# Performance work log

Measured on AMD Instinct MI355X. Metric: run time of the kernel, lower is better.

## Reference

```python
import jax, jax.numpy as jnp
import numpy as np

FP8_MAX = 448.0   # torch.finfo(float8_e4m3fn).max
BLK = 128         # block_size = [128, 128] for weights; [1, 128] for activations
E, H, I, T, TOPK = 8, 2048, 1408, 512, 2
FP8 = jnp.float8_e4m3fn


def fp8_round(x):
    """Round-trip through float8_e4m3fn (simulates .to(float8_e4m3fn))."""
    return jnp.clip(x, -FP8_MAX, FP8_MAX).astype(FP8).astype(jnp.float32)


def setup_inputs() -> dict:
    key = jax.random.key(0)
    ks = jax.random.split(key, 7)
    hidden_states = jax.random.normal(ks[0], (T, H), jnp.float32)
    top_k_index = jax.random.randint(ks[1], (T, TOPK), 0, E)
    top_k_weights = jax.random.uniform(ks[2], (T, TOPK), jnp.float32)
    # FP8 weight codes (stored as fp32 values exactly representable in e4m3fn)
    gate_up_proj = fp8_round(jax.random.normal(ks[3], (E, 2 * I, H), jnp.float32))
    gate_up_proj_scale_inv = jax.random.uniform(ks[4], (E, (2 * I) // BLK, H // BLK), jnp.float32, 1e-4, 1e-2)
    down_proj = fp8_round(jax.random.normal(ks[5], (E, H, I), jnp.float32))
    down_proj_scale_inv = jax.random.uniform(ks[6], (E, H // BLK, I // BLK), jnp.float32, 1e-4, 1e-2)
    return {
        "hidden_states": hidden_states,
        "top_k_index": top_k_index,
        "top_k_weights": top_k_weights,
        "gate_up_proj": gate_up_proj,
        "gate_up_proj_scale_inv": gate_up_proj_scale_inv,
        "down_proj": down_proj,
        "down_proj_scale_inv": down_proj_scale_inv,
    }


def dequant_weight(wq, s):
    # wq: [E, N, K] fp8 codes; s: [E, N//BLK, K//BLK] per-128x128-block scale_inv
    e, n, k = wq.shape
    wb = wq.reshape(e, n // BLK, BLK, k // BLK, BLK)
    return (wb * s[:, :, None, :, None]).reshape(e, n, k)


def quant_dequant_act(x):
    # dynamic per-(row, 128-block) fp8 activation quantization, then dequant
    shp = x.shape
    xb = x.reshape(shp[:-1] + (shp[-1] // BLK, BLK))
    amax = jnp.max(jnp.abs(xb), axis=-1, keepdims=True)
    scale = jnp.maximum(amax, 1e-12) / FP8_MAX
    q = fp8_round(xb / scale)
    return (q * scale).reshape(shp)


def reference(hidden_states, top_k_index, top_k_weights, gate_up_proj,
              gate_up_proj_scale_inv, down_proj, down_proj_scale_inv):
    w_gu = dequant_weight(gate_up_proj, gate_up_proj_scale_inv)  # [E, 2I, H]
    w_d = dequant_weight(down_proj, down_proj_scale_inv)         # [E, H, I]
    # activation quantization is per-token-block, so unrouted tokens are
    # unaffected; dense per-expert compute + combine-weight mask equals the
    # original gather/scatter loop exactly (unrouted contributions weight 0).
    x = quant_dequant_act(hidden_states)                         # [T, H]
    gate_up = jnp.einsum('th,enh->etn', x, w_gu)                 # [E, T, 2I]
    gate, up = jnp.split(gate_up, 2, axis=-1)
    h = jax.nn.silu(gate) * up                                   # [E, T, I]
    h = quant_dequant_act(h)
    down = jnp.einsum('eti,ehi->eth', h, w_d)                    # [E, T, H]
    # combine[t, e] = sum over top-k slots routing token t to expert e
    combine = jnp.sum(jax.nn.one_hot(top_k_index, E, dtype=top_k_weights.dtype)
                      * top_k_weights[..., None], axis=1)        # [T, E]
    out = jnp.einsum('eth,te->th', down, combine)
    return out.astype(hidden_states.dtype)
```

## Files before the change

kernel.cpp:

```cpp
#include <hip/hip_runtime.h>
#include <math.h>

#define NE 8
#define HD 2048
#define ID 1408
#define NT 512
#define FP8MAX 448.0f

typedef __attribute__((ext_vector_type(4))) float floatx4;

__device__ __forceinline__ floatx4 fzero4() {
    floatx4 z; z.x = 0.f; z.y = 0.f; z.z = 0.f; z.w = 0.f; return z;
}

#define OFF_OFFS  0
#define OFF_TOK   1024
#define OFF_WGT   8192
#define OFF_ENT   16384
#define OFF_XSG   32768
#define OFF_XG    131072
#define OFF_HS    (3*1024*1024)
#define OFF_HQ    (3*1024*1024 + 65536)
#define OFF_GU0   (5*1024*1024)
#define OFF_GU1   (17*1024*1024)

#define LDA 136

__global__ void route_kernel(const int* __restrict__ tki,
                             const float* __restrict__ tkw,
                             int* __restrict__ offs,
                             int* __restrict__ tok,
                             float* __restrict__ wgt,
                             int* __restrict__ ent) {
    __shared__ int cnt[NE];
    __shared__ int cur[NE];
    __shared__ int base[NE + 1];
    int tid = threadIdx.x;
    if (tid < NE) { cnt[tid] = 0; cur[tid] = 0; }
    __syncthreads();
    int e = tki[tid];
    atomicAdd(&cnt[e], 1);
    __syncthreads();
    if (tid == 0) {
        int s = 0;
        for (int i = 0; i < NE; i++) { base[i] = s; s += cnt[i]; }
        base[NE] = s;
    }
    __syncthreads();
    int pos = atomicAdd(&cur[e], 1);
    int j = base[e] + pos;
    tok[j] = tid >> 1;
    wgt[j] = tkw[tid];
    ent[tid] = j;
    if (tid <= NE) offs[tid] = base[tid];
}

__global__ void quant_x_kernel(const float* __restrict__ x,
                               const int* __restrict__ ent,
                               unsigned char* __restrict__ xg,
                               float* __restrict__ xsg) {
    int wid = (blockIdx.x * 256 + threadIdx.x) >> 6;
    int lane = threadIdx.x & 63;
    int t = wid >> 4;
    int b = wid & 15;
    const float2 v = *(const float2*)(x + (long)t * HD + b * 128 + lane * 2);
    float am = fmaxf(fabsf(v.x), fabsf(v.y));
    #pragma unroll
    for (int m = 32; m; m >>= 1) am = fmaxf(am, __shfl_xor(am, m));
    float scale = fmaxf(am, 1e-12f) / FP8MAX;
    int p = __builtin_amdgcn_cvt_pk_fp8_f32(v.x / scale, v.y / scale, 0, false);
    unsigned short pk = (unsigned short)(p & 0xffff);
    int e0 = ent[2 * t], e1 = ent[2 * t + 1];
    *(unsigned short*)(xg + (long)e0 * HD + b * 128 + lane * 2) = pk;
    *(unsigned short*)(xg + (long)e1 * HD + b * 128 + lane * 2) = pk;
    if (lane == 0) { xsg[e0 * 16 + b] = scale; xsg[e1 * 16 + b] = scale; }
}

__global__ void quant_h_kernel(const float* __restrict__ gu0,
                               const float* __restrict__ gu1,
                               unsigned char* __restrict__ hq,
                               float* __restrict__ hs) {
    int wid = (blockIdx.x * 256 + threadIdx.x) >> 6;
    int lane = threadIdx.x & 63;
    int j = wid / 11;
    int b = wid - j * 11;
    long base = (long)j * 2816 + b * 128 + lane * 2;
    float2 ga = *(const float2*)(gu0 + base);
    float2 gb = *(const float2*)(gu1 + base);
    float2 ua = *(const float2*)(gu0 + base + 1408);
    float2 ub = *(const float2*)(gu1 + base + 1408);
    float gx = ga.x + gb.x, gy = ga.y + gb.y;
    float ux = ua.x + ub.x, uy = ua.y + ub.y;
    float hx = (gx / (1.0f + expf(-gx))) * ux;
    float hy = (gy / (1.0f + expf(-gy))) * uy;
    float am = fmaxf(fabsf(hx), fabsf(hy));
    #pragma unroll
    for (int m = 32; m; m >>= 1) am = fmaxf(am, __shfl_xor(am, m));
    float scale = fmaxf(am, 1e-12f) / FP8MAX;
    int p = __builtin_amdgcn_cvt_pk_fp8_f32(hx / scale, hy / scale, 0, false);
    *(unsigned short*)(hq + (long)j * ID + b * 128 + lane * 2) =
        (unsigned short)(p & 0xffff);
    if (lane == 0) hs[j * 11 + b] = scale;
}

__global__ __launch_bounds__(256, 4) void gemm1_kernel(
    const unsigned char* __restrict__ xg,
    const float* __restrict__ xsg,
    const float* __restrict__ wgu,
    const float* __restrict__ sgu,
    const int* __restrict__ offs,
    float* __restrict__ gu0,
    float* __restrict__ gu1) {
    int e = blockIdx.z;
    int jb = blockIdx.x >> 1;
    int kh = blockIdx.x & 1;
    int o0 = offs[e], o1 = offs[e + 1];
    int ne = o1 - o0;
    if (ne <= 0) return;

    __shared__ __align__(16) unsigned char Asm[128 * LDA];
    __shared__ __align__(16) unsigned char Bsm[64 * LDA];
    __shared__ __align__(16) float sxa[128 * 20];

    int tid = threadIdx.x;
    int wave = tid >> 6;
    int lane = tid & 63;
    int lr = lane & 15;
    int lq = lane >> 4;

    int bcol = tid & 31;
    int brow0 = tid >> 5;
    const float* bG = wgu + ((long)e * 2816 + jb * 32 + brow0) * HD + bcol * 4;
    const float* bU = wgu + ((long)e * 2816 + 1408 + jb * 32 + brow0) * HD + bcol * 4;
    const float* sgp = sgu + (e * 22 + (jb >> 2)) * 16;
    const float* sup = sgu + (e * 22 + 11 + (jb >> 2)) * 16;

    int aseg = tid & 7;
    int arow0 = tid >> 3;
    int kbS = kh * 8, kbE = kbS + 8;

    for (int m0 = 0; m0 < ne; m0 += 128) {
        int rem = ne - m0;
        int j0 = o0 + m0;

        {
            int r = tid >> 1, q = tid & 1;
            int j = j0 + r; if (j >= o1) j = o0;
            float4 s0 = *(const float4*)(xsg + j * 16 + q * 8);
            float4 s1 = *(const float4*)(xsg + j * 16 + q * 8 + 4);
            *(float4*)&sxa[r * 20 + q * 8] = s0;
            *(float4*)&sxa[r * 20 + q * 8 + 4] = s1;
        }

        const unsigned char* aBase0;
        const unsigned char* aBase1;
        const unsigned char* aBase2;
        const unsigned char* aBase3;
        {
            int j;
            j = j0 + arow0;       if (j >= o1) j = o0; aBase0 = xg + (long)j * HD + aseg * 16;
            j = j0 + 32 + arow0;  if (j >= o1) j = o0; aBase1 = xg + (long)j * HD + aseg * 16;
            j = j0 + 64 + arow0;  if (j >= o1) j = o0; aBase2 = xg + (long)j * HD + aseg * 16;
            j = j0 + 96 + arow0;  if (j >= o1) j = o0; aBase3 = xg + (long)j * HD + aseg * 16;
        }

        floatx4 facc[8];
        #pragma unroll
        for (int i = 0; i < 8; i++) facc[i] = fzero4();

        for (int kb = kbS; kb < kbE; kb++) {
            {
                uint4 a0 = *(const uint4*)(aBase0 + kb * 128);
                uint4 a1 = *(const uint4*)(aBase1 + kb * 128);
                uint4 a2 = *(const uint4*)(aBase2 + kb * 128);
                uint4 a3 = *(const uint4*)(aBase3 + kb * 128);
                float4 f0 = *(const float4*)(bG + kb * 128);
                float4 f1 = *(const float4*)(bG + kb * 128 + 8 * HD);
                float4 f2 = *(const float4*)(bG + kb * 128 + 16 * HD);
                float4 f3 = *(const float4*)(bG + kb * 128 + 24 * HD);
                float4 f4 = *(const float4*)(bU + kb * 128);
                float4 f5 = *(const float4*)(bU + kb * 128 + 8 * HD);
                float4 f6 = *(const float4*)(bU + kb * 128 + 16 * HD);
                float4 f7 = *(const float4*)(bU + kb * 128 + 24 * HD);
                *(uint4*)(&Asm[(arow0)      * LDA + aseg * 16]) = a0;
                *(uint4*)(&Asm[(arow0 + 32) * LDA + aseg * 16]) = a1;
                *(uint4*)(&Asm[(arow0 + 64) * LDA + aseg * 16]) = a2;
                *(uint4*)(&Asm[(arow0 + 96) * LDA + aseg * 16]) = a3;
                int p0 = __builtin_amdgcn_cvt_pk_fp8_f32(f0.x, f0.y, 0, false);
                p0 = __builtin_amdgcn_cvt_pk_fp8_f32(f0.z, f0.w, p0, true);
                int p1 = __builtin_amdgcn_cvt_pk_fp8_f32(f1.x, f1.y, 0, false);
                p1 = __builtin_amdgcn_cvt_pk_fp8_f32(f1.z, f1.w, p1, true);
                int p2 = __builtin_amdgcn_cvt_pk_fp8_f32(f2.x, f2.y, 0, false);
                p2 = __builtin_amdgcn_cvt_pk_fp8_f32(f2.z, f2.w, p2, true);
                int p3 = __builtin_amdgcn_cvt_pk_fp8_f32(f3.x, f3.y, 0, false);
                p3 = __builtin_amdgcn_cvt_pk_fp8_f32(f3.z, f3.w, p3, true);
                int p4 = __builtin_amdgcn_cvt_pk_fp8_f32(f4.x, f4.y, 0, false);
                p4 = __builtin_amdgcn_cvt_pk_fp8_f32(f4.z, f4.w, p4, true);
                int p5 = __builtin_amdgcn_cvt_pk_fp8_f32(f5.x, f5.y, 0, false);
                p5 = __builtin_amdgcn_cvt_pk_fp8_f32(f5.z, f5.w, p5, true);
                int p6 = __builtin_amdgcn_cvt_pk_fp8_f32(f6.x, f6.y, 0, false);
                p6 = __builtin_amdgcn_cvt_pk_fp8_f32(f6.z, f6.w, p6, true);
                int p7 = __builtin_amdgcn_cvt_pk_fp8_f32(f7.x, f7.y, 0, false);
                p7 = __builtin_amdgcn_cvt_pk_fp8_f32(f7.z, f7.w, p7, true);
                *(unsigned int*)(&Bsm[(brow0)      * LDA + bcol * 4]) = (unsigned int)p0;
                *(unsigned int*)(&Bsm[(brow0 + 8)  * LDA + bcol * 4]) = (unsigned int)p1;
                *(unsigned int*)(&Bsm[(brow0 + 16) * LDA + bcol * 4]) = (unsigned int)p2;
                *(unsigned int*)(&Bsm[(brow0 + 24) * LDA + bcol * 4]) = (unsigned int)p3;
                *(unsigned int*)(&Bsm[(brow0 + 32) * LDA + bcol * 4]) = (unsigned int)p4;
                *(unsigned int*)(&Bsm[(brow0 + 40) * LDA + bcol * 4]) = (unsigned int)p5;
                *(unsigned int*)(&Bsm[(brow0 + 48) * LDA + bcol * 4]) = (unsigned int)p6;
                *(unsigned int*)(&Bsm[(brow0 + 56) * LDA + bcol * 4]) = (unsigned int)p7;
            }
            __syncthreads();
            floatx4 cacc[8];
            #pragma unroll
            for (int i = 0; i < 8; i++) cacc[i] = fzero4();
            #pragma unroll
            for (int ks = 0; ks < 4; ks++) {
                long a[2], b[4];
                #pragma unroll
                for (int mi = 0; mi < 2; mi++)
                    a[mi] = *(const long*)(&Asm[(wave * 32 + mi * 16 + lr) * LDA + ks * 32 + lq * 8]);
                #pragma unroll
                for (int ni = 0; ni < 4; ni++)
                    b[ni] = *(const long*)(&Bsm[(ni * 16 + lr) * LDA + ks * 32 + lq * 8]);
                #pragma unroll
                for (int mi = 0; mi < 2; mi++)
                    #pragma unroll
                    for (int ni = 0; ni < 4; ni++)
                        cacc[mi * 4 + ni] = __builtin_amdgcn_mfma_f32_16x16x32_fp8_fp8(
                            a[mi], b[ni], cacc[mi * 4 + ni], 0, 0, 0);
            }
            float sg = sgp[kb];
            float su = sup[kb];
            #pragma unroll
            for (int mi = 0; mi < 2; mi++) {
                #pragma unroll
                for (int reg = 0; reg < 4; reg++) {
                    float sx = sxa[(wave * 32 + mi * 16 + lq * 4 + reg) * 20 + kb];
                    #pragma unroll
                    for (int ni = 0; ni < 4; ni++) {
                        float sw = (ni < 2) ? sg : su;
                        facc[mi * 4 + ni][reg] += cacc[mi * 4 + ni][reg] * (sw * sx);
                    }
                }
            }
            __syncthreads();
        }

        float* gu = kh ? gu1 : gu0;
        #pragma unroll
        for (int mi = 0; mi < 2; mi++) {
            #pragma unroll
            for (int ni = 0; ni < 4; ni++) {
                #pragma unroll
                for (int reg = 0; reg < 4; reg++) {
                    int r = wave * 32 + mi * 16 + lq * 4 + reg;
                    if (r < rem) {
                        long base = (long)(j0 + r) * 2816;
                        long col = (ni < 2) ? (jb * 32 + ni * 16 + lr)
                                            : (1408 + jb * 32 + (ni - 2) * 16 + lr);
                        gu[base + col] = facc[mi * 4 + ni][reg];
                    }
                }
            }
        }
    }
}

__global__ __launch_bounds__(256, 4) void gemm2_kernel(
    const unsigned char* __restrict__ hq,
    const float* __restrict__ hs,
    const float* __restrict__ wd,
    const float* __restrict__ sd,
    const int* __restrict__ offs,
    float* __restrict__ d0,
    float* __restrict__ d1) {
    int e = blockIdx.z;
    int jb = blockIdx.x >> 1;
    int kh = blockIdx.x & 1;
    int o0 = offs[e], o1 = offs[e + 1];
    int ne = o1 - o0;
    if (ne <= 0) return;

    __shared__ __align__(16) unsigned char Asm[128 * LDA];
    __shared__ __align__(16) unsigned char Bsm[32 * LDA];
    __shared__ __align__(16) float sha[128 * 12];

    int tid = threadIdx.x;
    int wave = tid >> 6;
    int lane = tid & 63;
    int lr = lane & 15;
    int lq = lane >> 4;

    int aseg = tid & 7;
    int arow0 = tid >> 3;

    int bcol = tid & 31;
    int brow0 = tid >> 5;
    const float* bB = wd + ((long)e * HD + jb * 32 + brow0) * ID + bcol * 4;
    const float* sdp = sd + (e * 16 + (jb >> 2)) * 11;

    int kb0 = kh ? 6 : 0, kb1 = kh ? 11 : 6;
    float* dp = kh ? d1 : d0;

    for (int m0 = 0; m0 < ne; m0 += 128) {
        int rem = ne - m0;
        int j0 = o0 + m0;

        if (tid < 128) {
            int j = j0 + tid;
            if (j >= o1) j = o0;
            const float* s = hs + j * 11;
            #pragma unroll
            for (int k = 0; k < 11; k++) sha[tid * 12 + k] = s[k];
        }

        const unsigned char* aBase0;
        const unsigned char* aBase1;
        const unsigned char* aBase2;
        const unsigned char* aBase3;
        {
            int j;
            j = j0 + arow0;       if (j >= o1) j = o0; aBase0 = hq + (long)j * ID + aseg * 16;
            j = j0 + 32 + arow0;  if (j >= o1) j = o0; aBase1 = hq + (long)j * ID + aseg * 16;
            j = j0 + 64 + arow0;  if (j >= o1) j = o0; aBase2 = hq + (long)j * ID + aseg * 16;
            j = j0 + 96 + arow0;  if (j >= o1) j = o0; aBase3 = hq + (long)j * ID + aseg * 16;
        }

        floatx4 facc[4];
        #pragma unroll
        for (int i = 0; i < 4; i++) facc[i] = fzero4();

        for (int kb = kb0; kb < kb1; kb++) {
            {
                uint4 a0 = *(const uint4*)(aBase0 + kb * 128);
                uint4 a1 = *(const uint4*)(aBase1 + kb * 128);
                uint4 a2 = *(const uint4*)(aBase2 + kb * 128);
                uint4 a3 = *(const uint4*)(aBase3 + kb * 128);
                float4 f0 = *(const float4*)(bB + kb * 128);
                float4 f1 = *(const float4*)(bB + kb * 128 + 8 * ID);
                float4 f2 = *(const float4*)(bB + kb * 128 + 16 * ID);
                float4 f3 = *(const float4*)(bB + kb * 128 + 24 * ID);
                *(uint4*)(&Asm[(arow0)      * LDA + aseg * 16]) = a0;
                *(uint4*)(&Asm[(arow0 + 32) * LDA + aseg * 16]) = a1;
                *(uint4*)(&Asm[(arow0 + 64) * LDA + aseg * 16]) = a2;
                *(uint4*)(&Asm[(arow0 + 96) * LDA + aseg * 16]) = a3;
                int p0 = __builtin_amdgcn_cvt_pk_fp8_f32(f0.x, f0.y, 0, false);
                p0 = __builtin_amdgcn_cvt_pk_fp8_f32(f0.z, f0.w, p0, true);
                int p1 = __builtin_amdgcn_cvt_pk_fp8_f32(f1.x, f1.y, 0, false);
                p1 = __builtin_amdgcn_cvt_pk_fp8_f32(f1.z, f1.w, p1, true);
                int p2 = __builtin_amdgcn_cvt_pk_fp8_f32(f2.x, f2.y, 0, false);
                p2 = __builtin_amdgcn_cvt_pk_fp8_f32(f2.z, f2.w, p2, true);
                int p3 = __builtin_amdgcn_cvt_pk_fp8_f32(f3.x, f3.y, 0, false);
                p3 = __builtin_amdgcn_cvt_pk_fp8_f32(f3.z, f3.w, p3, true);
                *(unsigned int*)(&Bsm[(brow0)      * LDA + bcol * 4]) = (unsigned int)p0;
                *(unsigned int*)(&Bsm[(brow0 + 8)  * LDA + bcol * 4]) = (unsigned int)p1;
                *(unsigned int*)(&Bsm[(brow0 + 16) * LDA + bcol * 4]) = (unsigned int)p2;
                *(unsigned int*)(&Bsm[(brow0 + 24) * LDA + bcol * 4]) = (unsigned int)p3;
            }
            __syncthreads();
            floatx4 cacc[4];
            #pragma unroll
            for (int i = 0; i < 4; i++) cacc[i] = fzero4();
            #pragma unroll
            for (int ks = 0; ks < 4; ks++) {
                long a[2], b[2];
                #pragma unroll
                for (int mi = 0; mi < 2; mi++)
                    a[mi] = *(const long*)(&Asm[(wave * 32 + mi * 16 + lr) * LDA + ks * 32 + lq * 8]);
                #pragma unroll
                for (int ni = 0; ni < 2; ni++)
                    b[ni] = *(const long*)(&Bsm[(ni * 16 + lr) * LDA + ks * 32 + lq * 8]);
                #pragma unroll
                for (int mi = 0; mi < 2; mi++)
                    #pragma unroll
                    for (int ni = 0; ni < 2; ni++)
                        cacc[mi * 2 + ni] = __builtin_amdgcn_mfma_f32_16x16x32_fp8_fp8(
                            a[mi], b[ni], cacc[mi * 2 + ni], 0, 0, 0);
            }
            float sw = sdp[kb];
            #pragma unroll
            for (int mi = 0; mi < 2; mi++) {
                #pragma unroll
                for (int reg = 0; reg < 4; reg++) {
                    float sh = sha[(wave * 32 + mi * 16 + lq * 4 + reg) * 12 + kb];
                    #pragma unroll
                    for (int ni = 0; ni < 2; ni++)
                        facc[mi * 2 + ni][reg] += cacc[mi * 2 + ni][reg] * (sw * sh);
                }
            }
            __syncthreads();
        }

        #pragma unroll
        for (int mi = 0; mi < 2; mi++) {
            #pragma unroll
            for (int ni = 0; ni < 2; ni++) {
                #pragma unroll
                for (int reg = 0; reg < 4; reg++) {
                    int r = wave * 32 + mi * 16 + lq * 4 + reg;
                    if (r < rem) {
                        dp[(long)(j0 + r) * HD + jb * 32 + ni * 16 + lr] =
                            facc[mi * 2 + ni][reg];
                    }
                }
            }
        }
    }
}

__global__ void combine_kernel(const float* __restrict__ d0,
                               const float* __restrict__ d1,
                               const int* __restrict__ ent,
                               const float* __restrict__ tkw,
                               float* __restrict__ out) {
    int gid = blockIdx.x * 256 + threadIdx.x;
    int t = gid >> 9;
    int c4 = gid & 511;
    int j0 = ent[2 * t], j1 = ent[2 * t + 1];
    float w0 = tkw[2 * t], w1 = tkw[2 * t + 1];
    long b0 = (long)j0 * HD + c4 * 4;
    long b1 = (long)j1 * HD + c4 * 4;
    float4 a0 = *(const float4*)(d0 + b0);
    float4 a1 = *(const float4*)(d1 + b0);
    float4 a2 = *(const float4*)(d0 + b1);
    float4 a3 = *(const float4*)(d1 + b1);
    float4 r;
    r.x = w0 * (a0.x + a1.x) + w1 * (a2.x + a3.x);
    r.y = w0 * (a0.y + a1.y) + w1 * (a2.y + a3.y);
    r.z = w0 * (a0.z + a1.z) + w1 * (a2.z + a3.z);
    r.w = w0 * (a0.w + a1.w) + w1 * (a2.w + a3.w);
    *(float4*)(out + (long)t * HD + c4 * 4) = r;
}

extern "C" void kernel_launch(void* const* d_in, const int* in_sizes, int n_in,
                              void* d_out, int out_size, void* d_ws, size_t ws_size,
                              hipStream_t stream) {
    (void)in_sizes; (void)n_in; (void)out_size; (void)ws_size;
    const float* x   = (const float*)d_in[0];
    const int*   tki = (const int*)d_in[1];
    const float* tkw = (const float*)d_in[2];
    const float* wgu = (const float*)d_in[3];
    const float* sgu = (const float*)d_in[4];
    const float* wd  = (const float*)d_in[5];
    const float* sd  = (const float*)d_in[6];
    float* out = (float*)d_out;
    char* ws = (char*)d_ws;

    int*   offs = (int*)(ws + OFF_OFFS);
    int*   tok  = (int*)(ws + OFF_TOK);
    float* wgt  = (float*)(ws + OFF_WGT);
    int*   ent  = (int*)(ws + OFF_ENT);
    float* xsg  = (float*)(ws + OFF_XSG);
    unsigned char* xg = (unsigned char*)(ws + OFF_XG);
    float* hs   = (float*)(ws + OFF_HS);
    unsigned char* hq = (unsigned char*)(ws + OFF_HQ);
    float* gu0  = (float*)(ws + OFF_GU0);
    float* gu1  = (float*)(ws + OFF_GU1);
    float* dp0  = (float*)(ws + OFF_GU0);
    float* dp1  = (float*)(ws + OFF_GU1);

    route_kernel<<<1, 1024, 0, stream>>>(tki, tkw, offs, tok, wgt, ent);
    quant_x_kernel<<<2048, 256, 0, stream>>>(x, ent, xg, xsg);
    gemm1_kernel<<<dim3(88, 1, NE), 256, 0, stream>>>(xg, xsg, wgu, sgu, offs, gu0, gu1);
    quant_h_kernel<<<2816, 256, 0, stream>>>(gu0, gu1, hq, hs);
    gemm2_kernel<<<dim3(128, 1, NE), 256, 0, stream>>>(hq, hs, wd, sd, offs, dp0, dp1);
    combine_kernel<<<1024, 256, 0, stream>>>(dp0, dp1, ent, tkw, out);
}
```

Measured before the change: 381.3 us.

## Parallelize MoE GEMMs over M tiles and split gemm1 K into four partials

The per-expert M-tile loop in both GEMMs becomes a grid dimension (blockIdx.y, up to 3 tiles), so each block handles one 128-row tile. gemm1 also splits K into four parts instead of two and writes four partial buffers, which quant_h then sums. The aim is more concurrent blocks on the GPU, since the grid was only 88x8 or 128x8 with serial M loops. In exchange there is more partial-sum traffic to and from memory, blocks with no rows exit early, and gemm2's launch bound is raised to 5 blocks per CU.

Result: slower. 418.6 us (+9.8%).

```diff
diff --git a/kernel.cpp b/kernel.cpp
--- a/kernel.cpp
+++ b/kernel.cpp
@@ -21,10 +21,12 @@
 #define OFF_XG    131072
 #define OFF_HS    (3*1024*1024)
 #define OFF_HQ    (3*1024*1024 + 65536)
-#define OFF_GU0   (5*1024*1024)
-#define OFF_GU1   (17*1024*1024)
+#define OFF_GU    (5L*1024*1024)
+#define OFF_D0    (52L*1024*1024)
+#define OFF_D1    (61L*1024*1024)
 
 #define LDA 136
+#define GUQ (1024L * 2816)
 
 __global__ void route_kernel(const int* __restrict__ tki,
                              const float* __restrict__ tkw,
@@ -76,8 +78,7 @@
     if (lane == 0) { xsg[e0 * 16 + b] = scale; xsg[e1 * 16 + b] = scale; }
 }
 
-__global__ void quant_h_kernel(const float* __restrict__ gu0,
-                               const float* __restrict__ gu1,
+__global__ void quant_h_kernel(const float* __restrict__ gu,
                                unsigned char* __restrict__ hq,
                                float* __restrict__ hs) {
     int wid = (blockIdx.x * 256 + threadIdx.x) >> 6;
@@ -85,12 +86,13 @@
     int j = wid / 11;
     int b = wid - j * 11;
     long base = (long)j * 2816 + b * 128 + lane * 2;
-    float2 ga = *(const float2*)(gu0 + base);
-    float2 gb = *(const float2*)(gu1 + base);
-    float2 ua = *(const float2*)(gu0 + base + 1408);
-    float2 ub = *(const float2*)(gu1 + base + 1408);
-    float gx = ga.x + gb.x, gy = ga.y + gb.y;
-    float ux = ua.x + ub.x, uy = ua.y + ub.y;
+    float gx = 0.f, gy = 0.f, ux = 0.f, uy = 0.f;
+    #pragma unroll
+    for (int q = 0; q < 4; q++) {
+        float2 g = *(const float2*)(gu + q * GUQ + base);
+        float2 u = *(const float2*)(gu + q * GUQ + base + 1408);
+        gx += g.x; gy += g.y; ux += u.x; uy += u.y;
+    }
     float hx = (gx / (1.0f + expf(-gx))) * ux;
     float hy = (gy / (1.0f + expf(-gy))) * uy;
     float am = fmaxf(fabsf(hx), fabsf(hy));
@@ -109,24 +111,50 @@
     const float* __restrict__ wgu,
     const float* __restrict__ sgu,
     const int* __restrict__ offs,
-    float* __restrict__ gu0,
-    float* __restrict__ gu1) {
+    float* __restrict__ guB) {
     int e = blockIdx.z;
-    int jb = blockIdx.x >> 1;
-    int kh = blockIdx.x & 1;
+    int mt = blockIdx.y;
+    int jb = blockIdx.x >> 2;
+    int kq = blockIdx.x & 3;
     int o0 = offs[e], o1 = offs[e + 1];
     int ne = o1 - o0;
-    if (ne <= 0) return;
+    int m0 = mt * 128;
+    if (m0 >= ne) return;
+    int rem = ne - m0;
+    int j0 = o0 + m0;
 
     __shared__ __align__(16) unsigned char Asm[128 * LDA];
     __shared__ __align__(16) unsigned char Bsm[64 * LDA];
     __shared__ __align__(16) float sxa[128 * 20];
 
     int tid = threadIdx.x;
+    {
+        int r = tid >> 1, q = tid & 1;
+        int j = j0 + r; if (j >= o1) j = o0;
+        float4 s0 = *(const float4*)(xsg + j * 16 + q * 8);
+        float4 s1 = *(const float4*)(xsg + j * 16 + q * 8 + 4);
+        *(float4*)&sxa[r * 20 + q * 8] = s0;
+        *(float4*)&sxa[r * 20 + q * 8 + 4] = s1;
+    }
+
     int wave = tid >> 6;
     int lane = tid & 63;
     int lr = lane & 15;
     int lq = lane >> 4;
+
+    int aseg = tid & 7;
+    int arow0 = tid >> 3;
+    const unsigned char* aBase0;
+    const unsigned char* aBase1;
+    const unsigned char* aBase2;
+    const unsigned char* aBase3;
+    {
+        int j;
+        j = j0 + arow0;       if (j >= o1) j = o0; aBase0 = xg + (long)j * HD + aseg * 16;
+        j = j0 + 32 + arow0;  if (j >= o1) j = o0; aBase1 = xg + (long)j * HD + aseg * 16;
+        j = j0 + 64 + arow0;  if (j >= o1) j = o0; aBase2 = xg + (long)j * HD + aseg * 16;
+        j = j0 + 96 + arow0;  if (j >= o1) j = o0; aBase3 = xg + (long)j * HD + aseg * 16;
+    }
 
     int bcol = tid & 31;
     int brow0 = tid >> 5;
@@ -135,140 +163,112 @@
     const float* sgp = sgu + (e * 22 + (jb >> 2)) * 16;
     const float* sup = sgu + (e * 22 + 11 + (jb >> 2)) * 16;
 
-    int aseg = tid & 7;
-    int arow0 = tid >> 3;
-    int kbS = kh * 8, kbE = kbS + 8;
-
-    for (int m0 = 0; m0 < ne; m0 += 128) {
-        int rem = ne - m0;
-        int j0 = o0 + m0;
-
+    floatx4 facc[8];
+    #pragma unroll
+    for (int i = 0; i < 8; i++) facc[i] = fzero4();
+
+    int kbS = kq * 4, kbE = kbS + 4;
+
+    for (int kb = kbS; kb < kbE; kb++) {
         {
-            int r = tid >> 1, q = tid & 1;
-            int j = j0 + r; if (j >= o1) j = o0;
-            float4 s0 = *(const float4*)(xsg + j * 16 + q * 8);
-            float4 s1 = *(const float4*)(xsg + j * 16 + q * 8 + 4);
-            *(float4*)&sxa[r * 20 + q * 8] = s0;
-            *(float4*)&sxa[r * 20 + q * 8 + 4] = s1;
-        }
-
-        const unsigned char* aBase0;
-        const unsigned char* aBase1;
-        const unsigned char* aBase2;
-        const unsigned char* aBase3;
-        {
-            int j;
-            j = j0 + arow0;       if (j >= o1) j = o0; aBase0 = xg + (long)j * HD + aseg * 16;
-            j = j0 + 32 + arow0;  if (j >= o1) j = o0; aBase1 = xg + (long)j * HD + aseg * 16;
-            j = j0 + 64 + arow0;  if (j >= o1) j = o0; aBase2 = xg + (long)j * HD + aseg * 16;
-            j = j0 + 96 + arow0;  if (j >= o1) j = o0; aBase3 = xg + (long)j * HD + aseg * 16;
-        }
-
-        floatx4 facc[8];
-        #pragma unroll
-        for (int i = 0; i < 8; i++) facc[i] = fzero4();
-
-        for (int kb = kbS; kb < kbE; kb++) {
-            {
-                uint4 a0 = *(const uint4*)(aBase0 + kb * 128);
-                uint4 a1 = *(const uint4*)(aBase1 + kb * 128);
-                uint4 a2 = *(const uint4*)(aBase2 + kb * 128);
-                uint4 a3 = *(const uint4*)(aBase3 + kb * 128);
-                float4 f0 = *(const float4*)(bG + kb * 128);
-                float4 f1 = *(const float4*)(bG + kb * 128 + 8 * HD);
-                float4 f2 = *(const float4*)(bG + kb * 128 + 16 * HD);
-                float4 f3 = *(const float4*)(bG + kb * 128 + 24 * HD);
-                float4 f4 = *(const float4*)(bU + kb * 128);
-                float4 f5 = *(const float4*)(bU + kb * 128 + 8 * HD);
-                float4 f6 = *(const float4*)(bU + kb * 128 + 16 * HD);
-                float4 f7 = *(const float4*)(bU + kb * 128 + 24 * HD);
-                *(uint4*)(&Asm[(arow0)      * LDA + aseg * 16]) = a0;
-                *(uint4*)(&Asm[(arow0 + 32) * LDA + aseg * 16]) = a1;
-                *(uint4*)(&Asm[(arow0 + 64) * LDA + aseg * 16]) = a2;
-                *(uint4*)(&Asm[(arow0 + 96) * LDA + aseg * 16]) = a3;
-                int p0 = __builtin_amdgcn_cvt_pk_fp8_f32(f0.x, f0.y, 0, false);
-                p0 = __builtin_amdgcn_cvt_pk_fp8_f32(f0.z, f0.w, p0, true);
-                int p1 = __builtin_amdgcn_cvt_pk_fp8_f32(f1.x, f1.y, 0, false);
-                p1 = __builtin_amdgcn_cvt_pk_fp8_f32(f1.z, f1.w, p1, true);
-                int p2 = __builtin_amdgcn_cvt_pk_fp8_f32(f2.x, f2.y, 0, false);
-                p2 = __builtin_amdgcn_cvt_pk_fp8_f32(f2.z, f2.w, p2, true);
-                int p3 = __builtin_amdgcn_cvt_pk_fp8_f32(f3.x, f3.y, 0, false);
-                p3 = __builtin_amdgcn_cvt_pk_fp8_f32(f3.z, f3.w, p3, true);
-                int p4 = __builtin_amdgcn_cvt_pk_fp8_f32(f4.x, f4.y, 0, false);
-                p4 = __builtin_amdgcn_cvt_pk_fp8_f32(f4.z, f4.w, p4, true);
-                int p5 = __builtin_amdgcn_cvt_pk_fp8_f32(f5.x, f5.y, 0, false);
-                p5 = __builtin_amdgcn_cvt_pk_fp8_f32(f5.z, f5.w, p5, true);
-                int p6 = __builtin_amdgcn_cvt_pk_fp8_f32(f6.x, f6.y, 0, false);
-                p6 = __builtin_amdgcn_cvt_pk_fp8_f32(f6.z, f6.w, p6, true);
-                int p7 = __builtin_amdgcn_cvt_pk_fp8_f32(f7.x, f7.y, 0, false);
-                p7 = __builtin_amdgcn_cvt_pk_fp8_f32(f7.z, f7.w, p7, true);
-                *(unsigned int*)(&Bsm[(brow0)      * LDA + bcol * 4]) = (unsigned int)p0;
-                *(unsigned int*)(&Bsm[(brow0 + 8)  * LDA + bcol * 4]) = (unsigned int)p1;
-                *(unsigned int*)(&Bsm[(brow0 + 16) * LDA + bcol * 4]) = (unsigned int)p2;
-                *(unsigned int*)(&Bsm[(brow0 + 24) * LDA + bcol * 4]) = (unsigned int)p3;
-                *(unsigned int*)(&Bsm[(brow0 + 32) * LDA + bcol * 4]) = (unsigned int)p4;
-                *(unsigned int*)(&Bsm[(brow0 + 40) * LDA + bcol * 4]) = (unsigned int)p5;
-                *(unsigned int*)(&Bsm[(brow0 + 48) * LDA + bcol * 4]) = (unsigned int)p6;
-                *(unsigned int*)(&Bsm[(brow0 + 56) * LDA + bcol * 4]) = (unsigned int)p7;
-            }
-            __syncthreads();
-            floatx4 cacc[8];
-            #pragma unroll
-            for (int i = 0; i < 8; i++) cacc[i] = fzero4();
-            #pragma unroll
-            for (int ks = 0; ks < 4; ks++) {
-                long a[2], b[4];
-                #pragma unroll
-                for (int mi = 0; mi < 2; mi++)
-                    a[mi] = *(const long*)(&Asm[(wave * 32 + mi * 16 + lr) * LDA + ks * 32 + lq * 8]);
+            uint4 a0 = *(const uint4*)(aBase0 + kb * 128);
+            uint4 a1 = *(const uint4*)(aBase1 + kb * 128);
+            uint4 a2 = *(const uint4*)(aBase2 + kb * 128);
+            uint4 a3 = *(const uint4*)(aBase3 + kb * 128);
+            float4 f0 = *(const float4*)(bG + kb * 128);
+            float4 f1 = *(const float4*)(bG + kb * 128 + 8 * HD);
+            float4 f2 = *(const float4*)(bG + kb * 128 + 16 * HD);
+            float4 f3 = *(const float4*)(bG + kb * 128 + 24 * HD);
+            float4 f4 = *(const float4*)(bU + kb * 128);
+            float4 f5 = *(const float4*)(bU + kb * 128 + 8 * HD);
+            float4 f6 = *(const float4*)(bU + kb * 128 + 16 * HD);
+            float4 f7 = *(const float4*)(bU + kb * 128 + 24 * HD);
+            *(uint4*)(&Asm[(arow0)      * LDA + aseg * 16]) = a0;
+            *(uint4*)(&Asm[(arow0 + 32) * LDA + aseg * 16]) = a1;
+            *(uint4*)(&Asm[(arow0 + 64) * LDA + aseg * 16]) = a2;
+            *(uint4*)(&Asm[(arow0 + 96) * LDA + aseg * 16]) = a3;
+            int p0 = __builtin_amdgcn_cvt_pk_fp8_f32(f0.x, f0.y, 0, false);
+            p0 = __builtin_amdgcn_cvt_pk_fp8_f32(f0.z, f0.w, p0, true);
+            int p1 = __builtin_amdgcn_cvt_pk_fp8_f32(f1.x, f1.y, 0, false);
+            p1 = __builtin_amdgcn_cvt_pk_fp8_f32(f1.z, f1.w, p1, true);
+            int p2 = __builtin_amdgcn_cvt_pk_fp8_f32(f2.x, f2.y, 0, false);
+            p2 = __builtin_amdgcn_cvt_pk_fp8_f32(f2.z, f2.w, p2, true);
+            int p3 = __builtin_amdgcn_cvt_pk_fp8_f32(f3.x, f3.y, 0, false);
+            p3 = __builtin_amdgcn_cvt_pk_fp8_f32(f3.z, f3.w, p3, true);
+            int p4 = __builtin_amdgcn_cvt_pk_fp8_f32(f4.x, f4.y, 0, false);
+            p4 = __builtin_amdgcn_cvt_pk_fp8_f32(f4.z, f4.w, p4, true);
+            int p5 = __builtin_amdgcn_cvt_pk_fp8_f32(f5.x, f5.y, 0, false);
+            p5 = __builtin_amdgcn_cvt_pk_fp8_f32(f5.z, f5.w, p5, true);
+            int p6 = __builtin_amdgcn_cvt_pk_fp8_f32(f6.x, f6.y, 0, false);
+            p6 = __builtin_amdgcn_cvt_pk_fp8_f32(f6.z, f6.w, p6, true);
+            int p7 = __builtin_amdgcn_cvt_pk_fp8_f32(f7.x, f7.y, 0, false);
+            p7 = __builtin_amdgcn_cvt_pk_fp8_f32(f7.z, f7.w, p7, true);
+            *(unsigned int*)(&Bsm[(brow0)      * LDA + bcol * 4]) = (unsigned int)p0;
+            *(unsigned int*)(&Bsm[(brow0 + 8)  * LDA + bcol * 4]) = (unsigned int)p1;
+            *(unsigned int*)(&Bsm[(brow0 + 16) * LDA + bcol * 4]) = (unsigned int)p2;
+            *(unsigned int*)(&Bsm[(brow0 + 24) * LDA + bcol * 4]) = (unsigned int)p3;
+            *(unsigned int*)(&Bsm[(brow0 + 32) * LDA + bcol * 4]) = (unsigned int)p4;
+            *(unsigned int*)(&Bsm[(brow0 + 40) * LDA + bcol * 4]) = (unsigned int)p5;
+            *(unsigned int*)(&Bsm[(brow0 + 48) * LDA + bcol * 4]) = (unsigned int)p6;
+            *(unsigned int*)(&Bsm[(brow0 + 56) * LDA + bcol * 4]) = (unsigned int)p7;
+        }
+        __syncthreads();
+        floatx4 cacc[8];
+        #pragma unroll
+        for (int i = 0; i < 8; i++) cacc[i] = fzero4();
+        #pragma unroll
+        for (int ks = 0; ks < 4; ks++) {
+            long a[2], b[4];
+            #pragma unroll
+            for (int mi = 0; mi < 2; mi++)
+                a[mi] = *(const long*)(&Asm[(wave * 32 + mi * 16 + lr) * LDA + ks * 32 + lq * 8]);
+            #pragma unroll
+            for (int ni = 0; ni < 4; ni++)
+                b[ni] = *(const long*)(&Bsm[(ni * 16 + lr) * LDA + ks * 32 + lq * 8]);
+            #pragma unroll
+            for (int mi = 0; mi < 2; mi++)
                 #pragma unroll
                 for (int ni = 0; ni < 4; ni++)
-                    b[ni] = *(const long*)(&Bsm[(ni * 16 + lr) * LDA + ks * 32 + lq * 8]);
+                    cacc[mi * 4 + ni] = __builtin_amdgcn_mfma_f32_16x16x32_fp8_fp8(
+                        a[mi], b[ni], cacc[mi * 4 + ni], 0, 0, 0);
+        }
+        float sg = sgp[kb];
+        float su = sup[kb];
+        #pragma unroll
+        for (int mi = 0; mi < 2; mi++) {
+            #pragma unroll
+            for (int reg = 0; reg < 4; reg++) {
+                float sx = sxa[(wave * 32 + mi * 16 + lq * 4 + reg) * 20 + kb];
                 #pragma unroll
-                for (int mi = 0; mi < 2; mi++)
-                    #pragma unroll
-                    for (int ni = 0; ni < 4; ni++)
-                        cacc[mi * 4 + ni] = __builtin_amdgcn_mfma_f32_16x16x32_fp8_fp8(
-                            a[mi], b[ni], cacc[mi * 4 + ni], 0, 0, 0);
-            }
-            float sg = sgp[kb];
-            float su = sup[kb];
-            #pragma unroll
-            for (int mi = 0; mi < 2; mi++) {
-                #pragma unroll
-                for (int reg = 0; reg < 4; reg++) {
-                    float sx = sxa[(wave * 32 + mi * 16 + lq * 4 + reg) * 20 + kb];
-                    #pragma unroll
-                    for (int ni = 0; ni < 4; ni++) {
-                        float sw = (ni < 2) ? sg : su;
-                        facc[mi * 4 + ni][reg] += cacc[mi * 4 + ni][reg] * (sw * sx);
-                    }
+                for (int ni = 0; ni < 4; ni++) {
+                    float sw = (ni < 2) ? sg : su;
+                    facc[mi * 4 + ni][reg] += cacc[mi * 4 + ni][reg] * (sw * sx);
                 }
             }
-            __syncthreads();
-        }
-
-        float* gu = kh ? gu1 : gu0;
-        #pragma unroll
-        for (int mi = 0; mi < 2; mi++) {
-            #pragma unroll
-            for (int ni = 0; ni < 4; ni++) {
-                #pragma unroll
-                for (int reg = 0; reg < 4; reg++) {
-                    int r = wave * 32 + mi * 16 + lq * 4 + reg;
-                    if (r < rem) {
-                        long base = (long)(j0 + r) * 2816;
-                        long col = (ni < 2) ? (jb * 32 + ni * 16 + lr)
-                                            : (1408 + jb * 32 + (ni - 2) * 16 + lr);
-                        gu[base + col] = facc[mi * 4 + ni][reg];
-                    }
+        }
+        __syncthreads();
+    }
+
+    float* gu = guB + (long)kq * GUQ;
+    #pragma unroll
+    for (int mi = 0; mi < 2; mi++) {
+        #pragma unroll
+        for (int ni = 0; ni < 4; ni++) {
+            #pragma unroll
+            for (int reg = 0; reg < 4; reg++) {
+                int r = wave * 32 + mi * 16 + lq * 4 + reg;
+                if (r < rem) {
+                    long base = (long)(j0 + r) * 2816;
+                    long col = (ni < 2) ? (jb * 32 + ni * 16 + lr)
+                                        : (1408 + jb * 32 + (ni - 2) * 16 + lr);
+                    gu[base + col] = facc[mi * 4 + ni][reg];
                 }
             }
         }
     }
 }
 
-__global__ __launch_bounds__(256, 4) void gemm2_kernel(
+__global__ __launch_bounds__(256, 5) void gemm2_kernel(
     const unsigned char* __restrict__ hq,
     const float* __restrict__ hs,
     const float* __restrict__ wd,
@@ -277,17 +277,29 @@
     float* __restrict__ d0,
     float* __restrict__ d1) {
     int e = blockIdx.z;
+    int mt = blockIdx.y;
     int jb = blockIdx.x >> 1;
     int kh = blockIdx.x & 1;
     int o0 = offs[e], o1 = offs[e + 1];
     int ne = o1 - o0;
-    if (ne <= 0) return;
+    int m0 = mt * 128;
+    if (m0 >= ne) return;
+    int rem = ne - m0;
+    int j0 = o0 + m0;
 
     __shared__ __align__(16) unsigned char Asm[128 * LDA];
     __shared__ __align__(16) unsigned char Bsm[32 * LDA];
     __shared__ __align__(16) float sha[128 * 12];
 
     int tid = threadIdx.x;
+    if (tid < 128) {
+        int j = j0 + tid;
+        if (j >= o1) j = o0;
+        const float* s = hs + j * 11;
+        #pragma unroll
+        for (int k = 0; k < 11; k++) sha[tid * 12 + k] = s[k];
+    }
+
     int wave = tid >> 6;
     int lane = tid & 63;
     int lr = lane & 15;
@@ -295,115 +307,101 @@
 
     int aseg = tid & 7;
     int arow0 = tid >> 3;
+    const unsigned char* aBase0;
+    const unsigned char* aBase1;
+    const unsigned char* aBase2;
+    const unsigned char* aBase3;
+    {
+        int j;
+        j = j0 + arow0;       if (j >= o1) j = o0; aBase0 = hq + (long)j * ID + aseg * 16;
+        j = j0 + 32 + arow0;  if (j >= o1) j = o0; aBase1 = hq + (long)j * ID + aseg * 16;
+        j = j0 + 64 + arow0;  if (j >= o1) j = o0; aBase2 = hq + (long)j * ID + aseg * 16;
+        j = j0 + 96 + arow0;  if (j >= o1) j = o0; aBase3 = hq + (long)j * ID + aseg * 16;
+    }
 
     int bcol = tid & 31;
     int brow0 = tid >> 5;
     const float* bB = wd + ((long)e * HD + jb * 32 + brow0) * ID + bcol * 4;
     const float* sdp = sd + (e * 16 + (jb >> 2)) * 11;
 
+    floatx4 facc[4];
+    #pragma unroll
+    for (int i = 0; i < 4; i++) facc[i] = fzero4();
+
     int kb0 = kh ? 6 : 0, kb1 = kh ? 11 : 6;
-    float* dp = kh ? d1 : d0;
-
-    for (int m0 = 0; m0 < ne; m0 += 128) {
-        int rem = ne - m0;
-        int j0 = o0 + m0;
-
-        if (tid < 128) {
-            int j = j0 + tid;
-            if (j >= o1) j = o0;
-            const float* s = hs + j * 11;
-            #pragma unroll
-            for (int k = 0; k < 11; k++) sha[tid * 12 + k] = s[k];
-        }
-
-        const unsigned char* aBase0;
-        const unsigned char* aBase1;
-        const unsigned char* aBase2;
-        const unsigned char* aBase3;
+
+    for (int kb = kb0; kb < kb1; kb++) {
         {
-            int j;
-            j = j0 + arow0;       if (j >= o1) j = o0; aBase0 = hq + (long)j * ID + aseg * 16;
-            j = j0 + 32 + arow0;  if (j >= o1) j = o0; aBase1 = hq + (long)j * ID + aseg * 16;
-            j = j0 + 64 + arow0;  if (j >= o1) j = o0; aBase2 = hq + (long)j * ID + aseg * 16;
-            j = j0 + 96 + arow0;  if (j >= o1) j = o0; aBase3 = hq + (long)j * ID + aseg * 16;
-        }
-
-        floatx4 facc[4];
-        #pragma unroll
-        for (int i = 0; i < 4; i++) facc[i] = fzero4();
-
-        for (int kb = kb0; kb < kb1; kb++) {
-            {
-                uint4 a0 = *(const uint4*)(aBase0 + kb * 128);
-                uint4 a1 = *(const uint4*)(aBase1 + kb * 128);
-                uint4 a2 = *(const uint4*)(aBase2 + kb * 128);
-                uint4 a3 = *(const uint4*)(aBase3 + kb * 128);
-                float4 f0 = *(const float4*)(bB + kb * 128);
-                float4 f1 = *(const float4*)(bB + kb * 128 + 8 * ID);
-                float4 f2 = *(const float4*)(bB + kb * 128 + 16 * ID);
-                float4 f3 = *(const float4*)(bB + kb * 128 + 24 * ID);
-                *(uint4*)(&Asm[(arow0)      * LDA + aseg * 16]) = a0;
-                *(uint4*)(&Asm[(arow0 + 32) * LDA + aseg * 16]) = a1;
-                *(uint4*)(&Asm[(arow0 + 64) * LDA + aseg * 16]) = a2;
-                *(uint4*)(&Asm[(arow0 + 96) * LDA + aseg * 16]) = a3;
-                int p0 = __builtin_amdgcn_cvt_pk_fp8_f32(f0.x, f0.y, 0, false);
-                p0 = __builtin_amdgcn_cvt_pk_fp8_f32(f0.z, f0.w, p0, true);
-                int p1 = __builtin_amdgcn_cvt_pk_fp8_f32(f1.x, f1.y, 0, false);
-                p1 = __builtin_amdgcn_cvt_pk_fp8_f32(f1.z, f1.w, p1, true);
-                int p2 = __builtin_amdgcn_cvt_pk_fp8_f32(f2.x, f2.y, 0, false);
-                p2 = __builtin_amdgcn_cvt_pk_fp8_f32(f2.z, f2.w, p2, true);
-                int p3 = __builtin_amdgcn_cvt_pk_fp8_f32(f3.x, f3.y, 0, false);
-                p3 = __builtin_amdgcn_cvt_pk_fp8_f32(f3.z, f3.w, p3, true);
-                *(unsigned int*)(&Bsm[(brow0)      * LDA + bcol * 4]) = (unsigned int)p0;
-                *(unsigned int*)(&Bsm[(brow0 + 8)  * LDA + bcol * 4]) = (unsigned int)p1;
-                *(unsigned int*)(&Bsm[(brow0 + 16) * LDA + bcol * 4]) = (unsigned int)p2;
-                *(unsigned int*)(&Bsm[(brow0 + 24) * LDA + bcol * 4]) = (unsigned int)p3;
-            }
-            __syncthreads();
-            floatx4 cacc[4];
-            #pragma unroll
-            for (int i = 0; i < 4; i++) cacc[i] = fzero4();
-            #pragma unroll
-            for (int ks = 0; ks < 4; ks++) {
-                long a[2], b[2];
-                #pragma unroll
-                for (int mi = 0; mi < 2; mi++)
-                    a[mi] = *(const long*)(&Asm[(wave * 32 + mi * 16 + lr) * LDA + ks * 32 + lq * 8]);
+            uint4 a0 = *(const uint4*)(aBase0 + kb * 128);
+            uint4 a1 = *(const uint4*)(aBase1 + kb * 128);
+            uint4 a2 = *(const uint4*)(aBase2 + kb * 128);
+            uint4 a3 = *(const uint4*)(aBase3 + kb * 128);
+            float4 f0 = *(const float4*)(bB + kb * 128);
+            float4 f1 = *(const float4*)(bB + kb * 128 + 8 * ID);
+            float4 f2 = *(const float4*)(bB + kb * 128 + 16 * ID);
+            float4 f3 = *(const float4*)(bB + kb * 128 + 24 * ID);
+            *(uint4*)(&Asm[(arow0)      * LDA + aseg * 16]) = a0;
+            *(uint4*)(&Asm[(arow0 + 32) * LDA + aseg * 16]) = a1;
+            *(uint4*)(&Asm[(arow0 + 64) * LDA + aseg * 16]) = a2;
+            *(uint4*)(&Asm[(arow0 + 96) * LDA + aseg * 16]) = a3;
+            int p0 = __builtin_amdgcn_cvt_pk_fp8_f32(f0.x, f0.y, 0, false);
+            p0 = __builtin_amdgcn_cvt_pk_fp8_f32(f0.z, f0.w, p0, true);
+            int p1 = __builtin_amdgcn_cvt_pk_fp8_f32(f1.x, f1.y, 0, false);
+            p1 = __builtin_amdgcn_cvt_pk_fp8_f32(f1.z, f1.w, p1, true);
+            int p2 = __builtin_amdgcn_cvt_pk_fp8_f32(f2.x, f2.y, 0, false);
+            p2 = __builtin_amdgcn_cvt_pk_fp8_f32(f2.z, f2.w, p2, true);
+            int p3 = __builtin_amdgcn_cvt_pk_fp8_f32(f3.x, f3.y, 0, false);
+            p3 = __builtin_amdgcn_cvt_pk_fp8_f32(f3.z, f3.w, p3, true);
+            *(unsigned int*)(&Bsm[(brow0)      * LDA + bcol * 4]) = (unsigned int)p0;
+            *(unsigned int*)(&Bsm[(brow0 + 8)  * LDA + bcol * 4]) = (unsigned int)p1;
+            *(unsigned int*)(&Bsm[(brow0 + 16) * LDA + bcol * 4]) = (unsigned int)p2;
+            *(unsigned int*)(&Bsm[(brow0 + 24) * LDA + bcol * 4]) = (unsigned int)p3;
+        }
+        __syncthreads();
+        floatx4 cacc[4];
+        #pragma unroll
+        for (int i = 0; i < 4; i++) cacc[i] = fzero4();
+        #pragma unroll
+        for (int ks = 0; ks < 4; ks++) {
+            long a[2], b[2];
+            #pragma unroll
+            for (int mi = 0; mi < 2; mi++)
+                a[mi] = *(const long*)(&Asm[(wave * 32 + mi * 16 + lr) * LDA + ks * 32 + lq * 8]);
+            #pragma unroll
+            for (int ni = 0; ni < 2; ni++)
+                b[ni] = *(const long*)(&Bsm[(ni * 16 + lr) * LDA + ks * 32 + lq * 8]);
+            #pragma unroll
+            for (int mi = 0; mi < 2; mi++)
                 #pragma unroll
                 for (int ni = 0; ni < 2; ni++)
-                    b[ni] = *(const long*)(&Bsm[(ni * 16 + lr) * LDA + ks * 32 + lq * 8]);
+                    cacc[mi * 2 + ni] = __builtin_amdgcn_mfma_f32_16x16x32_fp8_fp8(
+                        a[mi], b[ni], cacc[mi * 2 + ni], 0, 0, 0);
+        }
+        float sw = sdp[kb];
+        #pragma unroll
+        for (int mi = 0; mi < 2; mi++) {
+            #pragma unroll
+            for (int reg = 0; reg < 4; reg++) {
+                float sh = sha[(wave * 32 + mi * 16 + lq * 4 + reg) * 12 + kb];
                 #pragma unroll
-                for (int mi = 0; mi < 2; mi++)
-                    #pragma unroll
-                    for (int ni = 0; ni < 2; ni++)
-                        cacc[mi * 2 + ni] = __builtin_amdgcn_mfma_f32_16x16x32_fp8_fp8(
-                            a[mi], b[ni], cacc[mi * 2 + ni], 0, 0, 0);
+                for (int ni = 0; ni < 2; ni++)
+                    facc[mi * 2 + ni][reg] += cacc[mi * 2 + ni][reg] * (sw * sh);
             }
-            float sw = sdp[kb];
-            #pragma unroll
-            for (int mi = 0; mi < 2; mi++) {
-                #pragma unroll
-                for (int reg = 0; reg < 4; reg++) {
-                    float sh = sha[(wave * 32 + mi * 16 + lq * 4 + reg) * 12 + kb];
-                    #pragma unroll
-                    for (int ni = 0; ni < 2; ni++)
-                        facc[mi * 2 + ni][reg] += cacc[mi * 2 + ni][reg] * (sw * sh);
-                }
-            }
-            __syncthreads();
-        }
-
-        #pragma unroll
-        for (int mi = 0; mi < 2; mi++) {
-            #pragma unroll
-            for (int ni = 0; ni < 2; ni++) {
-                #pragma unroll
-                for (int reg = 0; reg < 4; reg++) {
-                    int r = wave * 32 + mi * 16 + lq * 4 + reg;
-                    if (r < rem) {
-                        dp[(long)(j0 + r) * HD + jb * 32 + ni * 16 + lr] =
-                            facc[mi * 2 + ni][reg];
-                    }
+        }
+        __syncthreads();
+    }
+
+    float* dp = kh ? d1 : d0;
+    #pragma unroll
+    for (int mi = 0; mi < 2; mi++) {
+        #pragma unroll
+        for (int ni = 0; ni < 2; ni++) {
+            #pragma unroll
+            for (int reg = 0; reg < 4; reg++) {
+                int r = wave * 32 + mi * 16 + lq * 4 + reg;
+                if (r < rem) {
+                    dp[(long)(j0 + r) * HD + jb * 32 + ni * 16 + lr] =
+                        facc[mi * 2 + ni][reg];
                 }
             }
         }
@@ -456,15 +454,14 @@
     unsigned char* xg = (unsigned char*)(ws + OFF_XG);
     float* hs   = (float*)(ws + OFF_HS);
     unsigned char* hq = (unsigned char*)(ws + OFF_HQ);
-    float* gu0  = (float*)(ws + OFF_GU0);
-    float* gu1  = (float*)(ws + OFF_GU1);
-    float* dp0  = (float*)(ws + OFF_GU0);
-    float* dp1  = (float*)(ws + OFF_GU1);
+    float* guB  = (float*)(ws + OFF_GU);
+    float* dp0  = (float*)(ws + OFF_D0);
+    float* dp1  = (float*)(ws + OFF_D1);
 
     route_kernel<<<1, 1024, 0, stream>>>(tki, tkw, offs, tok, wgt, ent);
     quant_x_kernel<<<2048, 256, 0, stream>>>(x, ent, xg, xsg);
-    gemm1_kernel<<<dim3(88, 1, NE), 256, 0, stream>>>(xg, xsg, wgu, sgu, offs, gu0, gu1);
-    quant_h_kernel<<<2816, 256, 0, stream>>>(gu0, gu1, hq, hs);
-    gemm2_kernel<<<dim3(128, 1, NE), 256, 0, stream>>>(hq, hs, wd, sd, offs, dp0, dp1);
+    gemm1_kernel<<<dim3(176, 3, NE), 256, 0, stream>>>(xg, xsg, wgu, sgu, offs, guB);
+    quant_h_kernel<<<2816, 256, 0, stream>>>(guB, hq, hs);
+    gemm2_kernel<<<dim3(128, 3, NE), 256, 0, stream>>>(hq, hs, wd, sd, offs, dp0, dp1);
     combine_kernel<<<1024, 256, 0, stream>>>(dp0, dp1, ent, tkw, out);
 }
```
